# Performance work log

Hardware: AMD Instinct MI355X
Metric: run time of the kernel (lower is better)

## Reference

```python
import jax, jax.numpy as jnp
import numpy as np

N_NODES = 50000
N_EDGES = 600000
F_IN = 57
HID = 128
NEG_SLOPE = 0.2  # PyG GATConv default leaky_relu slope


def setup_inputs() -> dict:
    key = jax.random.key(0)
    ks = jax.random.split(key, 10)
    s = lambda k, shape, fan: jax.random.normal(k, shape, jnp.float32) / np.float32(np.sqrt(fan))
    x = jax.random.normal(ks[0], (N_NODES, F_IN), jnp.float32)
    edge_index = jax.random.randint(ks[1], (2, N_EDGES), 0, N_NODES)
    return {
        "x": x,
        "edge_index": edge_index,
        # layer1: GATConv(57 -> 128, heads=1)
        "W_gat": s(ks[2], (F_IN, HID), F_IN),
        "a_src": s(ks[3], (HID,), HID),
        "a_dst": s(ks[4], (HID,), HID),
        "b_gat": jnp.zeros((HID,), jnp.float32),
        # layer2: SAGEConv(128 -> 128, aggr='mean'): lin_l (with bias) on aggregated, lin_r (no bias) on self
        "W_l": s(ks[5], (HID, HID), HID),
        "b_l": jnp.zeros((HID,), jnp.float32),
        "W_r": s(ks[6], (HID, HID), HID),
        # layer3: Linear(128 -> 1)
        "W_out": s(ks[7], (HID, 1), HID),
        "b_out": jnp.zeros((1,), jnp.float32),
    }


def _gat_conv(x, src, dst, W, a_s, a_d, b, n):
    # PyG GATConv (heads=1): adds self-loops, attention softmax over incoming edges per dst node.
    loop = jnp.arange(n)
    src = jnp.concatenate([src, loop])
    dst = jnp.concatenate([dst, loop])
    h = x @ W                                   # [N, H]
    logit = jax.nn.leaky_relu((h @ a_s)[src] + (h @ a_d)[dst], NEG_SLOPE)  # [E+N]
    lmax = jax.lax.stop_gradient(jax.ops.segment_max(logit, dst, num_segments=n))
    ex = jnp.exp(logit - lmax[dst])
    denom = jax.ops.segment_sum(ex, dst, num_segments=n)
    alpha = ex / denom[dst]
    out = jax.ops.segment_sum(alpha[:, None] * h[src], dst, num_segments=n)  # [N, H]
    return out + b


def _sage_conv_mean(x, src, dst, W_l, b_l, W_r, n):
    # PyG SAGEConv: out = lin_l(mean_{j->i} x_j) + lin_r(x_i); no self-loops.
    msum = jax.ops.segment_sum(x[src], dst, num_segments=n)          # [N, H]
    cnt = jax.ops.segment_sum(jnp.ones_like(src, jnp.float32), dst, num_segments=n)
    mean = msum / jnp.maximum(cnt, 1.0)[:, None]
    return mean @ W_l + b_l + x @ W_r


def reference(x, edge_index, W_gat, a_src, a_dst, b_gat, W_l, b_l, W_r, W_out, b_out):
    n = x.shape[0]
    src, dst = edge_index[0], edge_index[1]
    h = jax.nn.relu(_gat_conv(x, src, dst, W_gat, a_src, a_dst, b_gat, n))
    h = jax.nn.relu(_sage_conv_mean(h, src, dst, W_l, b_l, W_r, n))
    return jax.nn.sigmoid(h @ W_out + b_out)  # [N, 1]
```

## Files before the change

### kernel.cpp

```cpp
#include <hip/hip_runtime.h>

#define NN 50000
#define NE 600000
#define F_IN 57
#define HID 128
#define NEG 0.2f
#define NB_SCAN ((NN + 255) / 256)

#define GIN_NODES 64
#define NB_GIN ((NN + GIN_NODES - 1) / NN == 0 ? ((NN + GIN_NODES - 1) / GIN_NODES) : ((NN + GIN_NODES - 1) / GIN_NODES))
#undef NB_GIN
#define NB_GIN ((NN + GIN_NODES - 1) / GIN_NODES)
#define XST 68

#define DN_NODES 64
#define NB_DENSE ((NN + DN_NODES - 1) / DN_NODES)

typedef unsigned short bf16_t;
typedef __attribute__((ext_vector_type(8))) short bf16x8;
typedef __attribute__((ext_vector_type(4))) float f32x4;

__device__ __forceinline__ float leaky(float v) { return v >= 0.f ? v : NEG * v; }
__device__ __forceinline__ float bf2f(bf16_t u) { return __uint_as_float(((unsigned)u) << 16); }
__device__ __forceinline__ bf16_t f2bf(float f) {
    unsigned u = __float_as_uint(f);
    return (bf16_t)((u + 0x7FFFu + ((u >> 16) & 1u)) >> 16);
}

__global__ __launch_bounds__(256) void k_gat_in(
    const float* __restrict__ x, const float* __restrict__ Wg,
    const float* __restrict__ a_s, const float* __restrict__ a_d,
    bf16_t* __restrict__ h, float* __restrict__ hs, float* __restrict__ hd) {
    __shared__ float WgS[F_IN * HID];
    __shared__ float xsT[F_IN][XST];
    int tid = threadIdx.x;
    int node0 = blockIdx.x * GIN_NODES;
    {
        const float4* g = (const float4*)Wg;
        float4* s = (float4*)WgS;
        for (int i = tid; i < F_IN * HID / 4; i += 256) s[i] = g[i];
    }
    for (int i = tid; i < GIN_NODES * F_IN; i += 256) {
        int n = i / F_IN;
        int k = i - n * F_IN;
        int gn = node0 + n;
        if (gn >= NN) gn = NN - 1;
        xsT[k][n] = x[gn * F_IN + k];
    }
    __syncthreads();

    int fq = tid & 31, nq = tid >> 5;
    int f0 = fq * 4, nb = nq * 8;
    float acc[8][4];
#pragma unroll
    for (int i = 0; i < 8; ++i)
#pragma unroll
        for (int j = 0; j < 4; ++j) acc[i][j] = 0.f;

    for (int k = 0; k < F_IN; ++k) {
        float4 w = *(const float4*)&WgS[k * HID + f0];
        float4 xa = *(const float4*)&xsT[k][nb];
        float4 xb = *(const float4*)&xsT[k][nb + 4];
        float xv[8] = {xa.x, xa.y, xa.z, xa.w, xb.x, xb.y, xb.z, xb.w};
        float wv[4] = {w.x, w.y, w.z, w.w};
#pragma unroll
        for (int i = 0; i < 8; ++i)
#pragma unroll
            for (int j = 0; j < 4; ++j)
                acc[i][j] = fmaf(xv[i], wv[j], acc[i][j]);
    }

    float4 as4 = *(const float4*)(a_s + f0);
    float4 ad4 = *(const float4*)(a_d + f0);
    float ps[8], pd[8];
#pragma unroll
    for (int i = 0; i < 8; ++i) {
        int gn = node0 + nb + i;
        if (gn < NN) {
            ushort4 hv;
            hv.x = f2bf(acc[i][0]); hv.y = f2bf(acc[i][1]);
            hv.z = f2bf(acc[i][2]); hv.w = f2bf(acc[i][3]);
            *(ushort4*)(h + (size_t)gn * HID + f0) = hv;
        }
        ps[i] = acc[i][0] * as4.x + acc[i][1] * as4.y + acc[i][2] * as4.z + acc[i][3] * as4.w;
        pd[i] = acc[i][0] * ad4.x + acc[i][1] * ad4.y + acc[i][2] * ad4.z + acc[i][3] * ad4.w;
    }
#pragma unroll
    for (int off = 16; off > 0; off >>= 1) {
#pragma unroll
        for (int i = 0; i < 8; ++i) {
            ps[i] += __shfl_xor(ps[i], off);
            pd[i] += __shfl_xor(pd[i], off);
        }
    }
    if (fq == 0) {
#pragma unroll
        for (int i = 0; i < 8; ++i) {
            int gn = node0 + nb + i;
            if (gn < NN) { hs[gn] = ps[i]; hd[gn] = pd[i]; }
        }
    }
}

__global__ __launch_bounds__(256) void k_pack_w(
    const float* __restrict__ Wl, const float* __restrict__ Wr, bf16_t* __restrict__ Bp) {
    int idx = blockIdx.x * 256 + threadIdx.x;
    if (idx >= 8 * 8 * 64) return;
    int lane = idx & 63;
    int kb = (idx >> 6) & 7;
    int nt = idx >> 9;
    int col = nt * 16 + (lane & 15);
    int kbase = kb * 32 + (lane >> 4) * 8;
    bf16_t v[8];
#pragma unroll
    for (int j = 0; j < 8; ++j) {
        int k = kbase + j;
        float w = (k < HID) ? Wl[k * HID + col] : Wr[(k - HID) * HID + col];
        v[j] = f2bf(w);
    }
    ushort4* o = (ushort4*)(Bp + (size_t)idx * 8);
    ushort4 lo, hi;
    lo.x = v[0]; lo.y = v[1]; lo.z = v[2]; lo.w = v[3];
    hi.x = v[4]; hi.y = v[5]; hi.z = v[6]; hi.w = v[7];
    o[0] = lo; o[1] = hi;
}

__global__ void k_hist(const int* __restrict__ dst, int* __restrict__ deg) {
    int e = blockIdx.x * blockDim.x + threadIdx.x;
    if (e < NE) atomicAdd(&deg[dst[e]], 1);
}

__global__ void k_scan1(const int* __restrict__ deg, int* __restrict__ rptr, int* __restrict__ bsum) {
    int t = threadIdx.x;
    int i = blockIdx.x * 256 + t;
    int v = (i < NN) ? deg[i] : 0;
    __shared__ int s[256];
    s[t] = v;
    __syncthreads();
    for (int off = 1; off < 256; off <<= 1) {
        int x = (t >= off) ? s[t - off] : 0;
        __syncthreads();
        s[t] += x;
        __syncthreads();
    }
    if (i < NN) rptr[i] = s[t] - v;
    if (t == 255) bsum[blockIdx.x] = s[255];
}

__global__ void k_scan3(int* __restrict__ rptr, const int* __restrict__ bsum) {
    int t = threadIdx.x;
    int v = (t < NB_SCAN && t < blockIdx.x) ? bsum[t] : 0;
#pragma unroll
    for (int off = 32; off > 0; off >>= 1) v += __shfl_xor(v, off);
    __shared__ int wsum[4];
    if ((t & 63) == 0) wsum[t >> 6] = v;
    __syncthreads();
    int pre = wsum[0] + wsum[1] + wsum[2] + wsum[3];
    int i = blockIdx.x * 256 + t;
    if (i < NN) rptr[i] += pre;
}

__global__ void k_fill(const int* __restrict__ src, const int* __restrict__ dst,
                       const int* __restrict__ rptr, int* __restrict__ fill,
                       int* __restrict__ esrc) {
    int e = blockIdx.x * blockDim.x + threadIdx.x;
    if (e >= NE) return;
    int d = dst[e];
    int pos = rptr[d] + atomicAdd(&fill[d], 1);
    esrc[pos] = src[e];
}

__global__ __launch_bounds__(128) void k_gat_agg(
    const int* __restrict__ rptr, const int* __restrict__ deg,
    const int* __restrict__ esrc, const float* __restrict__ hs,
    const float* __restrict__ hd, const bf16_t* __restrict__ h,
    const float* __restrict__ bg, bf16_t* __restrict__ h1) {
    int row = blockIdx.x;
    int t = threadIdx.x;
    int lane = t & 63, wid = t >> 6;
    int start = rptr[row];
    int dn = deg[row];
    int end = start + dn;
    float hdr = hd[row];
    float wself = __expf(leaky(hs[row] + hdr));

    __shared__ float ws[128];
    __shared__ int es[128];
    __shared__ float red[2];

    float denL = 0.f;
    float acc = wself * bf2f(h[(size_t)row * HID + t]);
    for (int c = start; c < end; c += 128) {
        int cl = min(128, end - c);
        __syncthreads();
        float w = 0.f;
        if (t < cl) {
            int s = esrc[c + t];
            es[t] = s;
            w = __expf(leaky(hs[s] + hdr));
            ws[t] = w;
        }
        denL += w;
        __syncthreads();
        int j = 0;
        for (; j + 4 <= cl; j += 4) {
            float w0 = ws[j], w1 = ws[j + 1], w2 = ws[j + 2], w3 = ws[j + 3];
            int s0 = es[j], s1 = es[j + 1], s2 = es[j + 2], s3 = es[j + 3];
            acc = fmaf(w0, bf2f(h[(size_t)s0 * HID + t]), acc);
            acc = fmaf(w1, bf2f(h[(size_t)s1 * HID + t]), acc);
            acc = fmaf(w2, bf2f(h[(size_t)s2 * HID + t]), acc);
            acc = fmaf(w3, bf2f(h[(size_t)s3 * HID + t]), acc);
        }
        for (; j < cl; ++j) acc = fmaf(ws[j], bf2f(h[(size_t)es[j] * HID + t]), acc);
    }
#pragma unroll
    for (int off = 32; off > 0; off >>= 1) denL += __shfl_xor(denL, off);
    __syncthreads();
    if (lane == 0) red[wid] = denL;
    __syncthreads();
    float den = wself + red[0] + red[1];

    float v = acc / den + bg[t];
    h1[(size_t)row * HID + t] = f2bf(v > 0.f ? v : 0.f);
}

__global__ __launch_bounds__(128) void k_sage_gather(
    const int* __restrict__ rptr, const int* __restrict__ deg,
    const int* __restrict__ esrc, const bf16_t* __restrict__ h1,
    bf16_t* __restrict__ mean) {
    int row = blockIdx.x;
    int t = threadIdx.x;
    int start = rptr[row];
    int dn = deg[row];
    int end = start + dn;
    float acc = 0.f;
    int e = start;
    for (; e + 4 <= end; e += 4) {
        int s0 = esrc[e], s1 = esrc[e + 1], s2 = esrc[e + 2], s3 = esrc[e + 3];
        float v0 = bf2f(h1[(size_t)s0 * HID + t]);
        float v1 = bf2f(h1[(size_t)s1 * HID + t]);
        float v2 = bf2f(h1[(size_t)s2 * HID + t]);
        float v3 = bf2f(h1[(size_t)s3 * HID + t]);
        acc += v0 + v1 + v2 + v3;
    }
    for (; e < end; ++e) acc += bf2f(h1[(size_t)esrc[e] * HID + t]);
    mean[(size_t)row * HID + t] = f2bf(acc / (float)(dn > 0 ? dn : 1));
}

__global__ __launch_bounds__(256) void k_dense_mfma(
    const bf16_t* __restrict__ mean, const bf16_t* __restrict__ h1,
    const bf16_t* __restrict__ Bp, const float* __restrict__ bl,
    const float* __restrict__ Wout, const float* __restrict__ bout,
    float* __restrict__ out) {
    int tid = threadIdx.x;
    int lane = tid & 63;
    int wv = tid >> 6;
    int node0 = blockIdx.x * DN_NODES + wv * 16;
    int arow = lane & 15;
    int kg = lane >> 4;
    int gn = node0 + arow;
    if (gn >= NN) gn = NN - 1;
    const bf16_t* mrow = mean + (size_t)gn * HID;
    const bf16_t* srow = h1 + (size_t)gn * HID;
    const bf16x8* bp = (const bf16x8*)Bp;

    f32x4 acc[8];
#pragma unroll
    for (int n = 0; n < 8; ++n) acc[n] = (f32x4){0.f, 0.f, 0.f, 0.f};

#pragma unroll
    for (int kb = 0; kb < 8; ++kb) {
        int k0 = kb * 32 + kg * 8;
        bf16x8 a = (kb < 4) ? *(const bf16x8*)(mrow + k0)
                            : *(const bf16x8*)(srow + (k0 - HID));
#pragma unroll
        for (int n = 0; n < 8; ++n) {
            bf16x8 b = bp[((n * 8 + kb) << 6) + lane];
            acc[n] = __builtin_amdgcn_mfma_f32_16x16x32_bf16(a, b, acc[n], 0, 0, 0);
        }
    }

    float pr[4] = {0.f, 0.f, 0.f, 0.f};
#pragma unroll
    for (int n = 0; n < 8; ++n) {
        int f = n * 16 + arow;
        float b = bl[f];
        float wo = Wout[f];
#pragma unroll
        for (int r = 0; r < 4; ++r) {
            float v = fmaxf(acc[n][r] + b, 0.f);
            pr[r] = fmaf(v, wo, pr[r]);
        }
    }
#pragma unroll
    for (int off = 8; off > 0; off >>= 1) {
#pragma unroll
        for (int r = 0; r < 4; ++r) pr[r] += __shfl_xor(pr[r], off);
    }
    if (arow == 0) {
        float bo = bout[0];
#pragma unroll
        for (int r = 0; r < 4; ++r) {
            int gno = node0 + kg * 4 + r;
            if (gno < NN) out[gno] = 1.f / (1.f + __expf(-(pr[r] + bo)));
        }
    }
}

extern "C" void kernel_launch(void* const* d_in, const int* in_sizes, int n_in,
                              void* d_out, int out_size, void* d_ws, size_t ws_size,
                              hipStream_t stream) {
    const float* x    = (const float*)d_in[0];
    const int*   ei   = (const int*)d_in[1];
    const float* Wg   = (const float*)d_in[2];
    const float* a_s  = (const float*)d_in[3];
    const float* a_d  = (const float*)d_in[4];
    const float* bg   = (const float*)d_in[5];
    const float* Wl   = (const float*)d_in[6];
    const float* bl   = (const float*)d_in[7];
    const float* Wr   = (const float*)d_in[8];
    const float* Wout = (const float*)d_in[9];
    const float* bout = (const float*)d_in[10];
    float* out = (float*)d_out;

    const int* src = ei;
    const int* dst = ei + NE;

    bf16_t* h    = (bf16_t*)d_ws;
    bf16_t* h1   = h + (size_t)NN * HID;
    bf16_t* mean = h1 + (size_t)NN * HID;
    bf16_t* Bp   = mean + (size_t)NN * HID;
    float* hs = (float*)(Bp + 8 * 8 * 64 * 8);
    float* hd = hs + NN;
    int* deg  = (int*)(hd + NN);
    int* fill = deg + NN;
    int* rptr = fill + NN;
    int* bsum = rptr + NN;
    int* esrc = bsum + NB_SCAN;

    hipMemsetAsync(deg, 0, (size_t)2 * NN * sizeof(int), stream);

    k_pack_w<<<16, 256, 0, stream>>>(Wl, Wr, Bp);
    k_gat_in<<<NB_GIN, 256, 0, stream>>>(x, Wg, a_s, a_d, h, hs, hd);

    k_hist<<<(NE + 255) / 256, 256, 0, stream>>>(dst, deg);
    k_scan1<<<NB_SCAN, 256, 0, stream>>>(deg, rptr, bsum);
    k_scan3<<<NB_SCAN, 256, 0, stream>>>(rptr, bsum);
    k_fill<<<(NE + 255) / 256, 256, 0, stream>>>(src, dst, rptr, fill, esrc);

    k_gat_agg<<<NN, 128, 0, stream>>>(rptr, deg, esrc, hs, hd, h, bg, h1);
    k_sage_gather<<<NN, 128, 0, stream>>>(rptr, deg, esrc, h1, mean);
    k_dense_mfma<<<NB_DENSE, 256, 0, stream>>>(mean, h1, Bp, bl, Wout, bout, out);
}
```

Measured before the change: 200.2 us.

## Vectorize GAT and SAGE edge gathers with 4-wide bf16 loads and edge splitting

Both gather kernels switch from one bf16 element per thread to ushort4 (4 bf16) loads per thread. Groups of 32 threads then cover a full 128-feature row, and several groups process different edges in parallel, with partial sums combined through shuffles and shared memory. The SAGE gather also packs two destination rows per block, and GAT stores pre-shifted byte offsets in shared memory. The aim is fewer, wider memory transactions and more gathers in flight per row, at the cost of extra reduction steps and idle lanes in the epilogue.

```diff
diff --git a/kernel.cpp b/kernel.cpp
--- a/kernel.cpp
+++ b/kernel.cpp
@@ -8,8 +8,6 @@
 #define NB_SCAN ((NN + 255) / 256)
 
 #define GIN_NODES 64
-#define NB_GIN ((NN + GIN_NODES - 1) / NN == 0 ? ((NN + GIN_NODES - 1) / GIN_NODES) : ((NN + GIN_NODES - 1) / GIN_NODES))
-#undef NB_GIN
 #define NB_GIN ((NN + GIN_NODES - 1) / GIN_NODES)
 #define XST 68
 
@@ -178,6 +176,8 @@
     int row = blockIdx.x;
     int t = threadIdx.x;
     int lane = t & 63, wid = t >> 6;
+    int sub = t >> 5;
+    int fq = t & 31;
     int start = rptr[row];
     int dn = deg[row];
     int end = start + dn;
@@ -187,64 +187,103 @@
     __shared__ float ws[128];
     __shared__ int es[128];
     __shared__ float red[2];
-
+    __shared__ __align__(16) float xr[32][4];
+
+    float a0 = 0.f, a1 = 0.f, a2 = 0.f, a3 = 0.f;
+    if (sub == 0) {
+        ushort4 hv = *(const ushort4*)(h + (size_t)row * HID + fq * 4);
+        a0 = wself * bf2f(hv.x); a1 = wself * bf2f(hv.y);
+        a2 = wself * bf2f(hv.z); a3 = wself * bf2f(hv.w);
+    }
     float denL = 0.f;
-    float acc = wself * bf2f(h[(size_t)row * HID + t]);
     for (int c = start; c < end; c += 128) {
         int cl = min(128, end - c);
         __syncthreads();
         float w = 0.f;
         if (t < cl) {
-            int s = esrc[c + t];
-            es[t] = s;
-            w = __expf(leaky(hs[s] + hdr));
+            int sn = esrc[c + t];
+            es[t] = sn << 8;
+            w = __expf(leaky(hs[sn] + hdr));
             ws[t] = w;
         }
         denL += w;
         __syncthreads();
-        int j = 0;
-        for (; j + 4 <= cl; j += 4) {
-            float w0 = ws[j], w1 = ws[j + 1], w2 = ws[j + 2], w3 = ws[j + 3];
-            int s0 = es[j], s1 = es[j + 1], s2 = es[j + 2], s3 = es[j + 3];
-            acc = fmaf(w0, bf2f(h[(size_t)s0 * HID + t]), acc);
-            acc = fmaf(w1, bf2f(h[(size_t)s1 * HID + t]), acc);
-            acc = fmaf(w2, bf2f(h[(size_t)s2 * HID + t]), acc);
-            acc = fmaf(w3, bf2f(h[(size_t)s3 * HID + t]), acc);
-        }
-        for (; j < cl; ++j) acc = fmaf(ws[j], bf2f(h[(size_t)es[j] * HID + t]), acc);
+        for (int j = sub; j < cl; j += 4) {
+            float wj = ws[j];
+            const bf16_t* hr = (const bf16_t*)((const char*)h + (size_t)(unsigned)es[j]) + fq * 4;
+            ushort4 hv = *(const ushort4*)hr;
+            a0 = fmaf(wj, bf2f(hv.x), a0);
+            a1 = fmaf(wj, bf2f(hv.y), a1);
+            a2 = fmaf(wj, bf2f(hv.z), a2);
+            a3 = fmaf(wj, bf2f(hv.w), a3);
+        }
     }
 #pragma unroll
     for (int off = 32; off > 0; off >>= 1) denL += __shfl_xor(denL, off);
+    if (lane == 0) red[wid] = denL;
+    a0 += __shfl_xor(a0, 32); a1 += __shfl_xor(a1, 32);
+    a2 += __shfl_xor(a2, 32); a3 += __shfl_xor(a3, 32);
+    if (wid == 1 && lane < 32) {
+        xr[lane][0] = a0; xr[lane][1] = a1; xr[lane][2] = a2; xr[lane][3] = a3;
+    }
     __syncthreads();
-    if (lane == 0) red[wid] = denL;
-    __syncthreads();
-    float den = wself + red[0] + red[1];
-
-    float v = acc / den + bg[t];
-    h1[(size_t)row * HID + t] = f2bf(v > 0.f ? v : 0.f);
+    if (wid == 0 && lane < 32) {
+        float den = wself + red[0] + red[1];
+        float inv = 1.f / den;
+        float4 xv = *(const float4*)xr[lane];
+        float4 b4 = *(const float4*)(bg + fq * 4);
+        float v0 = (a0 + xv.x) * inv + b4.x;
+        float v1 = (a1 + xv.y) * inv + b4.y;
+        float v2 = (a2 + xv.z) * inv + b4.z;
+        float v3 = (a3 + xv.w) * inv + b4.w;
+        ushort4 o;
+        o.x = f2bf(v0 > 0.f ? v0 : 0.f);
+        o.y = f2bf(v1 > 0.f ? v1 : 0.f);
+        o.z = f2bf(v2 > 0.f ? v2 : 0.f);
+        o.w = f2bf(v3 > 0.f ? v3 : 0.f);
+        *(ushort4*)(h1 + (size_t)row * HID + fq * 4) = o;
+    }
 }
 
 __global__ __launch_bounds__(128) void k_sage_gather(
     const int* __restrict__ rptr, const int* __restrict__ deg,
     const int* __restrict__ esrc, const bf16_t* __restrict__ h1,
     bf16_t* __restrict__ mean) {
-    int row = blockIdx.x;
     int t = threadIdx.x;
+    int wid = t >> 6;
+    int row = blockIdx.x * 2 + wid;
+    if (row >= NN) return;
+    int lane = t & 63;
+    int sub = (t >> 5) & 1;
+    int fq = t & 31;
     int start = rptr[row];
     int dn = deg[row];
     int end = start + dn;
-    float acc = 0.f;
-    int e = start;
-    for (; e + 4 <= end; e += 4) {
-        int s0 = esrc[e], s1 = esrc[e + 1], s2 = esrc[e + 2], s3 = esrc[e + 3];
-        float v0 = bf2f(h1[(size_t)s0 * HID + t]);
-        float v1 = bf2f(h1[(size_t)s1 * HID + t]);
-        float v2 = bf2f(h1[(size_t)s2 * HID + t]);
-        float v3 = bf2f(h1[(size_t)s3 * HID + t]);
-        acc += v0 + v1 + v2 + v3;
-    }
-    for (; e < end; ++e) acc += bf2f(h1[(size_t)esrc[e] * HID + t]);
-    mean[(size_t)row * HID + t] = f2bf(acc / (float)(dn > 0 ? dn : 1));
+    float a0 = 0.f, a1 = 0.f, a2 = 0.f, a3 = 0.f;
+    int e = start + sub;
+    for (; e + 2 < end; e += 4) {
+        const bf16_t* r0 = h1 + (size_t)esrc[e] * HID + fq * 4;
+        const bf16_t* r1 = h1 + (size_t)esrc[e + 2] * HID + fq * 4;
+        ushort4 u0 = *(const ushort4*)r0;
+        ushort4 u1 = *(const ushort4*)r1;
+        a0 += bf2f(u0.x) + bf2f(u1.x);
+        a1 += bf2f(u0.y) + bf2f(u1.y);
+        a2 += bf2f(u0.z) + bf2f(u1.z);
+        a3 += bf2f(u0.w) + bf2f(u1.w);
+    }
+    if (e < end) {
+        ushort4 u0 = *(const ushort4*)(h1 + (size_t)esrc[e] * HID + fq * 4);
+        a0 += bf2f(u0.x); a1 += bf2f(u0.y); a2 += bf2f(u0.z); a3 += bf2f(u0.w);
+    }
+    a0 += __shfl_xor(a0, 32); a1 += __shfl_xor(a1, 32);
+    a2 += __shfl_xor(a2, 32); a3 += __shfl_xor(a3, 32);
+    if (lane < 32) {
+        float inv = 1.f / (float)(dn > 0 ? dn : 1);
+        ushort4 o;
+        o.x = f2bf(a0 * inv); o.y = f2bf(a1 * inv);
+        o.z = f2bf(a2 * inv); o.w = f2bf(a3 * inv);
+        *(ushort4*)(mean + (size_t)row * HID + fq * 4) = o;
+    }
 }
 
 __global__ __launch_bounds__(256) void k_dense_mfma(
@@ -349,6 +388,6 @@
     k_fill<<<(NE + 255) / 256, 256, 0, stream>>>(src, dst, rptr, fill, esrc);
 
     k_gat_agg<<<NN, 128, 0, stream>>>(rptr, deg, esrc, hs, hd, h, bg, h1);
-    k_sage_gather<<<NN, 128, 0, stream>>>(rptr, deg, esrc, h1, mean);
+    k_sage_gather<<<(NN + 1) / 2, 128, 0, stream>>>(rptr, deg, esrc, h1, mean);
     k_dense_mfma<<<NB_DENSE, 256, 0, stream>>>(mean, h1, Bp, bl, Wout, bout, out);
 }
```

Result: no change. 197.8 us (-1.2%).

## Restructure GAT and SAGE gathers to one wavefront per node with vector loads

Applied to the files above, without the earlier changes.

Both neighbor-aggregation kernels now map one 64-lane wavefront per destination node, four nodes per block. Each lane loads 8 bf16 features at once, and four edge slots are processed in parallel and combined with cross-lane shuffles. This drops the shared-memory staging and block barriers in the GAT kernel, cuts the block count, and replaces scalar 2-byte gathers with 16-byte gathers. The cost is more registers per lane and idle slots on the tail of each node's edge list.

```diff
diff --git a/kernel.cpp b/kernel.cpp
--- a/kernel.cpp
+++ b/kernel.cpp
@@ -8,8 +8,6 @@
 #define NB_SCAN ((NN + 255) / 256)
 
 #define GIN_NODES 64
-#define NB_GIN ((NN + GIN_NODES - 1) / NN == 0 ? ((NN + GIN_NODES - 1) / GIN_NODES) : ((NN + GIN_NODES - 1) / GIN_NODES))
-#undef NB_GIN
 #define NB_GIN ((NN + GIN_NODES - 1) / GIN_NODES)
 #define XST 68
 
@@ -170,81 +168,135 @@
     esrc[pos] = src[e];
 }
 
-__global__ __launch_bounds__(128) void k_gat_agg(
+__global__ __launch_bounds__(256) void k_gat_agg(
     const int* __restrict__ rptr, const int* __restrict__ deg,
     const int* __restrict__ esrc, const float* __restrict__ hs,
     const float* __restrict__ hd, const bf16_t* __restrict__ h,
     const float* __restrict__ bg, bf16_t* __restrict__ h1) {
-    int row = blockIdx.x;
-    int t = threadIdx.x;
-    int lane = t & 63, wid = t >> 6;
+    int tid = threadIdx.x;
+    int row = blockIdx.x * 4 + (tid >> 6);
+    if (row >= NN) return;
+    int lane = tid & 63;
+    int slot = lane >> 4;
+    int f8 = lane & 15;
+
     int start = rptr[row];
     int dn = deg[row];
     int end = start + dn;
     float hdr = hd[row];
     float wself = __expf(leaky(hs[row] + hdr));
 
-    __shared__ float ws[128];
-    __shared__ int es[128];
-    __shared__ float red[2];
-
+    float a[8];
+#pragma unroll
+    for (int j = 0; j < 8; ++j) a[j] = 0.f;
     float denL = 0.f;
-    float acc = wself * bf2f(h[(size_t)row * HID + t]);
-    for (int c = start; c < end; c += 128) {
-        int cl = min(128, end - c);
-        __syncthreads();
-        float w = 0.f;
-        if (t < cl) {
-            int s = esrc[c + t];
-            es[t] = s;
-            w = __expf(leaky(hs[s] + hdr));
-            ws[t] = w;
-        }
+
+    if (slot == 0) {
+        bf16x8 r = *(const bf16x8*)(h + (size_t)row * HID + f8 * 8);
+#pragma unroll
+        for (int j = 0; j < 8; ++j) a[j] = wself * bf2f((bf16_t)r[j]);
+    }
+
+    int e = start;
+    for (; e + 8 <= end; e += 8) {
+        int s0 = esrc[e + slot];
+        int s1 = esrc[e + 4 + slot];
+        float w0 = __expf(leaky(hs[s0] + hdr));
+        float w1 = __expf(leaky(hs[s1] + hdr));
+        bf16x8 r0 = *(const bf16x8*)(h + (size_t)s0 * HID + f8 * 8);
+        bf16x8 r1 = *(const bf16x8*)(h + (size_t)s1 * HID + f8 * 8);
+        denL += w0 + w1;
+#pragma unroll
+        for (int j = 0; j < 8; ++j) {
+            a[j] = fmaf(w0, bf2f((bf16_t)r0[j]), a[j]);
+            a[j] = fmaf(w1, bf2f((bf16_t)r1[j]), a[j]);
+        }
+    }
+    for (; e < end; e += 4) {
+        int i = e + slot;
+        bool act = i < end;
+        int sn = esrc[act ? i : end - 1];
+        float w = act ? __expf(leaky(hs[sn] + hdr)) : 0.f;
+        bf16x8 r = *(const bf16x8*)(h + (size_t)sn * HID + f8 * 8);
         denL += w;
-        __syncthreads();
-        int j = 0;
-        for (; j + 4 <= cl; j += 4) {
-            float w0 = ws[j], w1 = ws[j + 1], w2 = ws[j + 2], w3 = ws[j + 3];
-            int s0 = es[j], s1 = es[j + 1], s2 = es[j + 2], s3 = es[j + 3];
-            acc = fmaf(w0, bf2f(h[(size_t)s0 * HID + t]), acc);
-            acc = fmaf(w1, bf2f(h[(size_t)s1 * HID + t]), acc);
-            acc = fmaf(w2, bf2f(h[(size_t)s2 * HID + t]), acc);
-            acc = fmaf(w3, bf2f(h[(size_t)s3 * HID + t]), acc);
-        }
-        for (; j < cl; ++j) acc = fmaf(ws[j], bf2f(h[(size_t)es[j] * HID + t]), acc);
-    }
-#pragma unroll
-    for (int off = 32; off > 0; off >>= 1) denL += __shfl_xor(denL, off);
-    __syncthreads();
-    if (lane == 0) red[wid] = denL;
-    __syncthreads();
-    float den = wself + red[0] + red[1];
-
-    float v = acc / den + bg[t];
-    h1[(size_t)row * HID + t] = f2bf(v > 0.f ? v : 0.f);
-}
-
-__global__ __launch_bounds__(128) void k_sage_gather(
+#pragma unroll
+        for (int j = 0; j < 8; ++j) a[j] = fmaf(w, bf2f((bf16_t)r[j]), a[j]);
+    }
+
+#pragma unroll
+    for (int j = 0; j < 8; ++j) {
+        a[j] += __shfl_xor(a[j], 16);
+        a[j] += __shfl_xor(a[j], 32);
+    }
+    denL += __shfl_xor(denL, 16);
+    denL += __shfl_xor(denL, 32);
+    float inv = 1.f / (wself + denL);
+
+    if (lane < 16) {
+        float4 b0 = *(const float4*)(bg + lane * 8);
+        float4 b1 = *(const float4*)(bg + lane * 8 + 4);
+        float bb[8] = {b0.x, b0.y, b0.z, b0.w, b1.x, b1.y, b1.z, b1.w};
+        bf16x8 o;
+#pragma unroll
+        for (int j = 0; j < 8; ++j) {
+            float v = a[j] * inv + bb[j];
+            o[j] = (short)f2bf(v > 0.f ? v : 0.f);
+        }
+        *(bf16x8*)(h1 + (size_t)row * HID + lane * 8) = o;
+    }
+}
+
+__global__ __launch_bounds__(256) void k_sage_gather(
     const int* __restrict__ rptr, const int* __restrict__ deg,
     const int* __restrict__ esrc, const bf16_t* __restrict__ h1,
     bf16_t* __restrict__ mean) {
-    int row = blockIdx.x;
-    int t = threadIdx.x;
+    int tid = threadIdx.x;
+    int row = blockIdx.x * 4 + (tid >> 6);
+    if (row >= NN) return;
+    int lane = tid & 63;
+    int slot = lane >> 4;
+    int f8 = lane & 15;
+
     int start = rptr[row];
     int dn = deg[row];
     int end = start + dn;
-    float acc = 0.f;
+
+    float a[8];
+#pragma unroll
+    for (int j = 0; j < 8; ++j) a[j] = 0.f;
+
     int e = start;
-    for (; e + 4 <= end; e += 4) {
-        int s0 = esrc[e], s1 = esrc[e + 1], s2 = esrc[e + 2], s3 = esrc[e + 3];
-        float v0 = bf2f(h1[(size_t)s0 * HID + t]);
-        float v1 = bf2f(h1[(size_t)s1 * HID + t]);
-        float v2 = bf2f(h1[(size_t)s2 * HID + t]);
-        float v3 = bf2f(h1[(size_t)s3 * HID + t]);
-        acc += v0 + v1 + v2 + v3;
-    }
-    for (; e < end; ++e) acc += bf2f(h1[(size_t)esrc[e] * HID + t]);
-    mean[(size_t)row * HID + t] = f2bf(acc / (float)(dn > 0 ? dn : 1));
+    for (; e + 8 <= end; e += 8) {
+        int s0 = esrc[e + slot];
+        int s1 = esrc[e + 4 + slot];
+        bf16x8 r0 = *(const bf16x8*)(h1 + (size_t)s0 * HID + f8 * 8);
+        bf16x8 r1 = *(const bf16x8*)(h1 + (size_t)s1 * HID + f8 * 8);
+#pragma unroll
+        for (int j = 0; j < 8; ++j)
+            a[j] += bf2f((bf16_t)r0[j]) + bf2f((bf16_t)r1[j]);
+    }
+    for (; e < end; e += 4) {
+        int i = e + slot;
+        bool act = i < end;
+        int sn = esrc[act ? i : end - 1];
+        bf16x8 r = *(const bf16x8*)(h1 + (size_t)sn * HID + f8 * 8);
+        float w = act ? 1.f : 0.f;
+#pragma unroll
+        for (int j = 0; j < 8; ++j) a[j] = fmaf(w, bf2f((bf16_t)r[j]), a[j]);
+    }
+
+#pragma unroll
+    for (int j = 0; j < 8; ++j) {
+        a[j] += __shfl_xor(a[j], 16);
+        a[j] += __shfl_xor(a[j], 32);
+    }
+    if (lane < 16) {
+        float inv = 1.f / (float)(dn > 0 ? dn : 1);
+        bf16x8 o;
+#pragma unroll
+        for (int j = 0; j < 8; ++j) o[j] = (short)f2bf(a[j] * inv);
+        *(bf16x8*)(mean + (size_t)row * HID + lane * 8) = o;
+    }
 }
 
 __global__ __launch_bounds__(256) void k_dense_mfma(
@@ -348,7 +400,7 @@
     k_scan3<<<NB_SCAN, 256, 0, stream>>>(rptr, bsum);
     k_fill<<<(NE + 255) / 256, 256, 0, stream>>>(src, dst, rptr, fill, esrc);
 
-    k_gat_agg<<<NN, 128, 0, stream>>>(rptr, deg, esrc, hs, hd, h, bg, h1);
-    k_sage_gather<<<NN, 128, 0, stream>>>(rptr, deg, esrc, h1, mean);
+    k_gat_agg<<<(NN + 3) / 4, 256, 0, stream>>>(rptr, deg, esrc, hs, hd, h, bg, h1);
+    k_sage_gather<<<(NN + 3) / 4, 256, 0, stream>>>(rptr, deg, esrc, h1, mean);
     k_dense_mfma<<<NB_DENSE, 256, 0, stream>>>(mean, h1, Bp, bl, Wout, bout, out);
 }
```

Result: faster. 170.7 us (-14.7%).
